# Performance work log

Measured on AMD Instinct MI355X. Metric: run time of the kernel, lower is better.

The kernel has to match this reference:

```python
import jax, jax.numpy as jnp
import numpy as np

# --- fixed model configuration (from init_kwargs) ---
Nx, Nu, Ny, Np = 3, 1, 2, 5
Nz = Np * (Ny + Nu)          # 15
F, V, DELTA = 0.1, 1.0, 1.0  # ps (flow), volume, sampling time
CAMEAN, CBMEAN = 0.5, 0.4    # yscale means
CASTD, CBSTD = 0.3, 0.2      # yscale stds
CAFMEAN, CAFSTD = 1.0, 0.5   # uscale


def _fnn(x, W1, b1, W2, b2):
    # dense(tanh) -> dense(linear), as createDenseLayers/fnnTf
    return jnp.tanh(x @ W1 + b1) @ W2 + b2


def setup_inputs() -> dict:
    B, T = 4096, 1024
    key = jax.random.key(0)
    ks = jax.random.split(key, 16)
    g = lambda k, shp, fan: (jax.random.normal(k, shp, jnp.float32) / np.sqrt(fan))
    return {
        "u": jax.random.normal(ks[0], (B, T, Nu), jnp.float32),
        "xz0": jax.random.normal(ks[1], (B, Nx + Nz), jnp.float32),
        "r1_W1": g(ks[2], (1, 16), 1),  "r1_b1": jnp.zeros((16,), jnp.float32),
        "r1_W2": g(ks[3], (16, 1), 16), "r1_b2": jnp.zeros((1,), jnp.float32),
        "r2_W1": g(ks[4], (2, 16), 2),  "r2_b1": jnp.zeros((16,), jnp.float32),
        "r2_W2": g(ks[5], (16, 1), 16), "r2_b2": jnp.zeros((1,), jnp.float32),
        "eC_W1": g(ks[6], (Nz, 32), Nz), "eC_b1": jnp.zeros((32,), jnp.float32),
        "eC_W2": g(ks[7], (32, 1), 32),  "eC_b2": jnp.zeros((1,), jnp.float32),
    }


def _forward(u, xz0, r1_W1, r1_b1, r1_W2, r1_b2,
             r2_W1, r2_b1, r2_W2, r2_b2, eC_W1, eC_b1, eC_W2, eC_b2):

    def fxu(x, uu):
        Ca, Cb, Cc = x[:, 0:1], x[:, 1:2], x[:, 2:3]
        Caf = uu[:, 0:1]
        r1 = _fnn(Ca, r1_W1, r1_b1, r1_W2, r1_b2) * CASTD
        r2 = _fnn(jnp.concatenate((Cb, Cc), -1), r2_W1, r2_b1, r2_W2, r2_b2) * CBSTD
        Ca = Ca * CASTD + CAMEAN
        Cb = Cb * CBSTD + CBMEAN
        Cc = Cc * CBSTD + CBMEAN
        Caf = Caf * CAFSTD + CAFMEAN
        dCa = F * (Caf - Ca) / V - r1
        dCb = -F * Cb / V + r1 - 3.0 * r2
        dCc = -F * Cc / V + r2
        return jnp.concatenate([dCa / CASTD, dCb / CBSTD, dCc / CBSTD], -1)

    # initial state: replace Cc with NN estimate from past data z0
    y0 = xz0[:, :Ny]
    z0 = xz0[:, Nx:]
    Cc0 = _fnn(z0, eC_W1, eC_b1, eC_W2, eC_b2)
    xz = jnp.concatenate((y0, Cc0, z0), -1)  # [B, Nx+Nz]

    def step(xz, uu):
        x, z = xz[:, :Nx], xz[:, Nx:]
        ypseq, upseq = z[:, :Np * Ny], z[:, Np * Ny:]
        k1 = fxu(x, uu)
        k2 = fxu(x + DELTA * (k1 / 2.0), uu)
        k3 = fxu(x + DELTA * (k2 / 2.0), uu)
        k4 = fxu(x + DELTA * k3, uu)
        xplus = x + (DELTA / 6.0) * (k1 + 2.0 * k2 + 2.0 * k3 + k4)
        zplus = jnp.concatenate((ypseq[:, Ny:], x[:, :Ny], upseq[:, Nu:], uu), -1)
        CcNN = _fnn(z, eC_W1, eC_b1, eC_W2, eC_b2)
        y = jnp.concatenate((x, CcNN), -1)  # [B, Nx+1]
        return jnp.concatenate((xplus, zplus), -1), y

    u_t = jnp.swapaxes(u, 0, 1)  # [T, B, Nu]
    _, ys = jax.lax.scan(step, xz, u_t)
    yseq_full = jnp.swapaxes(ys, 0, 1)      # [B, T, Nx+1]
    yseq = yseq_full[..., :Ny]
    xseq = yseq_full[..., :Nx]
    return yseq_full, yseq, xseq


def reference(u, xz0, r1_W1, r1_b1, r1_W2, r1_b2,
              r2_W1, r2_b1, r2_W2, r2_b2, eC_W1, eC_b1, eC_W2, eC_b2):
    return _forward(u, xz0, r1_W1, r1_b1, r1_W2, r1_b2,
                    r2_W1, r2_b1, r2_W2, r2_b2, eC_W1, eC_b1, eC_W2, eC_b2)
```

## Files before the change

kernel.cpp:

```cpp
#include <hip/hip_runtime.h>
#include <stdint.h>
#include <math.h>

#define NB 4096
#define NT 1024


#if __has_builtin(__builtin_amdgcn_exp2f)
#define EXP2F __builtin_amdgcn_exp2f
#else
#define EXP2F exp2f
#endif
#if __has_builtin(__builtin_amdgcn_rcpf)
#define RCPF __builtin_amdgcn_rcpf
#else
#define RCPF(x) (1.0f / (x))
#endif

#define TANH_SCALE 2.885390081777927f

template <int CTRL>
__device__ __forceinline__ float dppmov(float x) {
  return __int_as_float(
      __builtin_amdgcn_update_dpp(0, __float_as_int(x), CTRL, 0xF, 0xF, true));
}

__device__ __forceinline__ float quadred(float a) {
  a += dppmov<0xB1>(a);
  a += dppmov<0x4E>(a);
  return a;
}

__global__ __launch_bounds__(64) void phase1_kernel(
    const float* __restrict__ u, const float* __restrict__ xz0,
    const float* __restrict__ r1W1, const float* __restrict__ r1b1,
    const float* __restrict__ r1W2, const float* __restrict__ r1b2,
    const float* __restrict__ r2W1, const float* __restrict__ r2b1,
    const float* __restrict__ r2W2, const float* __restrict__ r2b2,
    const float* __restrict__ eCW1, const float* __restrict__ eCb1,
    const float* __restrict__ eCW2, const float* __restrict__ eCb2,
    float* __restrict__ out) {
  const int tid = threadIdx.x;
  const int cl = tid & 7;
  const int q = tid & 3;
  const bool isQ1 = (tid & 4) != 0;
  const int chain = (blockIdx.x << 3) + (tid >> 3);

  float wA[4], wB[4], wC[4], wPn2[4];
  float wPsum = 0.0f;
#pragma unroll
  for (int m = 0; m < 4; ++m) {
    const int un = q + 4 * m;
    float wp;
    if (!isQ1) {
      wA[m] = r1W1[un] * TANH_SCALE;
      wB[m] = 0.0f;
      wC[m] = r1b1[un] * TANH_SCALE;
      wp = r1W2[un];
    } else {
      wA[m] = r2W1[un] * TANH_SCALE;
      wB[m] = r2W1[16 + un] * TANH_SCALE;
      wC[m] = r2b1[un] * TANH_SCALE;
      wp = r2W2[un];
    }
    wPn2[m] = -2.0f * wp;
    wPsum += wp;
  }
  const float c1 = r1b2[0];
  const float c2 = r2b2[0];
  const float C0b = 1.0f / 6.0f - c1;
  const float C1 = -0.2f + 1.5f * c1 - 3.0f * c2;
  const float C2 = c2 - 0.2f;
  const float aO0 = isQ1 ? 0.0f : -1.0f;
  const float aT0 = isQ1 ? -1.0f : 0.0f;
  const float aO1 = isQ1 ? -3.0f : 1.5f;
  const float aT1 = isQ1 ? 1.5f : -3.0f;
  const float aO2 = isQ1 ? 1.0f : 0.0f;
  const float aT2 = isQ1 ? 0.0f : 1.0f;

  const float* xzr = xz0 + chain * 18;
  float x0 = xzr[0];
  float x1 = xzr[1];
  float x2;

  {
    float eh[4], ewn2[4];
    float ewsum = 0.0f;
#pragma unroll
    for (int m = 0; m < 4; ++m) {
      const int un = 4 * cl + m;
      eh[m] = eCb1[un];
      ewn2[m] = -2.0f * eCW2[un];
      ewsum += eCW2[un];
    }
#pragma unroll
    for (int i = 0; i < 15; ++i) {
      const float z = xzr[3 + i];
#pragma unroll
      for (int m = 0; m < 4; ++m)
        eh[m] = __builtin_fmaf(z, eCW1[i * 32 + 4 * cl + m], eh[m]);
    }
    float pl = ewsum;
#pragma unroll
    for (int m = 0; m < 4; ++m) {
      const float e = EXP2F(eh[m] * TANH_SCALE);
      const float r = RCPF(e + 1.0f);
      pl = __builtin_fmaf(ewn2[m], r, pl);
    }
    pl = quadred(pl);
    pl = pl + dppmov<0x141>(pl);
    x2 = pl + eCb2[0];
  }

  size_t idx0;
  int stride;
  if (cl < 3) {
    idx0 = (size_t)chain * NT * 4 + cl;
    stride = 4;
  } else if (cl < 5) {
    idx0 = (size_t)NB * NT * 4 + (size_t)chain * NT * 2 + (cl - 3);
    stride = 2;
  } else {
    idx0 = (size_t)NB * NT * 6 + (size_t)chain * NT * 3 + (cl - 5);
    stride = 3;
  }
  float* sp = out + idx0;
  const bool selx0 = (cl == 0) || (cl == 3) || (cl == 5);
  const bool selx1 = (cl == 1) || (cl == 4) || (cl == 6);

  auto fxu = [&](float s0s, float s1s, float s2s, float C0t, float& k0,
                 float& k1, float& k2) {
    const float sU = isQ1 ? s1s : s0s;
    const float sV = isQ1 ? s2s : s0s;
    float r[4];
#pragma unroll
    for (int m = 0; m < 4; ++m) {
      float h = __builtin_fmaf(sV, wB[m], wC[m]);
      h = __builtin_fmaf(sU, wA[m], h);
      const float e = EXP2F(h);
      r[m] = RCPF(e + 1.0f);
    }
    float pl = wPsum;
#pragma unroll
    for (int m = 0; m < 4; ++m) pl = __builtin_fmaf(wPn2[m], r[m], pl);
    const float Sown = quadred(pl);
    const float Soth = dppmov<0x141>(Sown);
    const float u0 = __builtin_fmaf(-0.1f, s0s, C0t);
    const float u1 = __builtin_fmaf(-0.1f, s1s, C1);
    const float u2 = __builtin_fmaf(-0.1f, s2s, C2);
    k0 = __builtin_fmaf(aO0, Sown, u0);
    k1 = __builtin_fmaf(aO1, Sown, u1);
    k2 = __builtin_fmaf(aO2, Sown, u2);
    k0 = __builtin_fmaf(aT0, Soth, k0);
    k1 = __builtin_fmaf(aT1, Soth, k1);
    k2 = __builtin_fmaf(aT2, Soth, k2);
  };

  const float* urow = u + (size_t)chain * NT;
  float4 ucur = *(const float4*)urow;
  for (int t4 = 0; t4 < NT; t4 += 4) {
    const int tn = (t4 + 4 < NT) ? (t4 + 4) : (NT - 4);
    const float4 unext = *(const float4*)(urow + tn);
    const float us[4] = {ucur.x, ucur.y, ucur.z, ucur.w};
#pragma unroll
    for (int e = 0; e < 4; ++e) {
      const float v = selx0 ? x0 : (selx1 ? x1 : x2);
      *sp = v;
      sp += stride;
      const float C0t = __builtin_fmaf(us[e], 1.0f / 6.0f, C0b);
      float k10, k11, k12, k20, k21, k22, k30, k31, k32, k40, k41, k42;
      fxu(x0, x1, x2, C0t, k10, k11, k12);
      fxu(__builtin_fmaf(0.5f, k10, x0), __builtin_fmaf(0.5f, k11, x1),
          __builtin_fmaf(0.5f, k12, x2), C0t, k20, k21, k22);
      fxu(__builtin_fmaf(0.5f, k20, x0), __builtin_fmaf(0.5f, k21, x1),
          __builtin_fmaf(0.5f, k22, x2), C0t, k30, k31, k32);
      fxu(x0 + k30, x1 + k31, x2 + k32, C0t, k40, k41, k42);
      float tA = k20 + k30;
      tA = __builtin_fmaf(2.0f, tA, k10) + k40;
      x0 = __builtin_fmaf(1.0f / 6.0f, tA, x0);
      float tB = k21 + k31;
      tB = __builtin_fmaf(2.0f, tB, k11) + k41;
      x1 = __builtin_fmaf(1.0f / 6.0f, tB, x1);
      float tC = k22 + k32;
      tC = __builtin_fmaf(2.0f, tC, k12) + k42;
      x2 = __builtin_fmaf(1.0f / 6.0f, tC, x2);
    }
    ucur = unext;
  }
}

__global__ __launch_bounds__(256) void phase2_kernel(
    const float* __restrict__ u, const float* __restrict__ xz0,
    const float* __restrict__ eCW1, const float* __restrict__ eCb1,
    const float* __restrict__ eCW2, const float* __restrict__ eCb2,
    float* __restrict__ out) {
  __shared__ float lw[32][16];
  __shared__ float lw2[32];
  const int tid = threadIdx.x;
  if (tid < 32) {
#pragma unroll
    for (int i = 0; i < 15; ++i) lw[tid][i] = eCW1[i * 32 + tid] * TANH_SCALE;
    lw[tid][15] = eCb1[tid] * TANH_SCALE;
    lw2[tid] = -2.0f * eCW2[tid];
  }
  __syncthreads();

  const int b = blockIdx.x;
  const int t0 = tid << 2;
  const float2* ysrow =
      (const float2*)(out + (size_t)NB * NT * 4) + (size_t)b * NT;
  const float* urow = u + (size_t)b * NT;
  const float* xzr = xz0 + b * 18;

  float yw[16], uw[8];
#pragma unroll
  for (int idx = 0; idx < 8; ++idx) {
    const int tp = t0 - 5 + idx;
    float a, c, uu;
    if (tp >= 0) {
      const float2 h = ysrow[tp];
      a = h.x;
      c = h.y;
      uu = urow[tp];
    } else {
      a = xzr[3 + 2 * (tp + 5)];
      c = xzr[4 + 2 * (tp + 5)];
      uu = xzr[13 + (tp + 5)];
    }
    yw[2 * idx] = a;
    yw[2 * idx + 1] = c;
    uw[idx] = uu;
  }

  float acc[4] = {0.f, 0.f, 0.f, 0.f};
  for (int j = 0; j < 32; ++j) {
    const float4 wa = ((const float4*)lw[j])[0];
    const float4 wb = ((const float4*)lw[j])[1];
    const float4 wc = ((const float4*)lw[j])[2];
    const float4 wd = ((const float4*)lw[j])[3];
    const float w2n = lw2[j];
#pragma unroll
    for (int e = 0; e < 4; ++e) {
      float h = wd.w;
      h = __builtin_fmaf(yw[2 * e + 0], wa.x, h);
      h = __builtin_fmaf(yw[2 * e + 1], wa.y, h);
      h = __builtin_fmaf(yw[2 * e + 2], wa.z, h);
      h = __builtin_fmaf(yw[2 * e + 3], wa.w, h);
      h = __builtin_fmaf(yw[2 * e + 4], wb.x, h);
      h = __builtin_fmaf(yw[2 * e + 5], wb.y, h);
      h = __builtin_fmaf(yw[2 * e + 6], wb.z, h);
      h = __builtin_fmaf(yw[2 * e + 7], wb.w, h);
      h = __builtin_fmaf(yw[2 * e + 8], wc.x, h);
      h = __builtin_fmaf(yw[2 * e + 9], wc.y, h);
      h = __builtin_fmaf(uw[e + 0], wc.z, h);
      h = __builtin_fmaf(uw[e + 1], wc.w, h);
      h = __builtin_fmaf(uw[e + 2], wd.x, h);
      h = __builtin_fmaf(uw[e + 3], wd.y, h);
      h = __builtin_fmaf(uw[e + 4], wd.z, h);
      const float r = RCPF(EXP2F(h) + 1.0f);
      acc[e] = __builtin_fmaf(w2n, r, acc[e]);
    }
  }
  float sw = 0.0f;
#pragma unroll
  for (int j = 0; j < 32; ++j) sw += eCW2[j];
  const float C = eCb2[0] + sw;
  float* yfrow = out + (size_t)b * NT * 4;
#pragma unroll
  for (int e = 0; e < 4; ++e) {
    yfrow[(t0 + e) * 4 + 3] = acc[e] + C;
  }
}

extern "C" void kernel_launch(void* const* d_in, const int* in_sizes, int n_in,
                              void* d_out, int out_size, void* d_ws,
                              size_t ws_size, hipStream_t stream) {
  const float* u = (const float*)d_in[0];
  const float* xz0 = (const float*)d_in[1];
  const float* r1W1 = (const float*)d_in[2];
  const float* r1b1 = (const float*)d_in[3];
  const float* r1W2 = (const float*)d_in[4];
  const float* r1b2 = (const float*)d_in[5];
  const float* r2W1 = (const float*)d_in[6];
  const float* r2b1 = (const float*)d_in[7];
  const float* r2W2 = (const float*)d_in[8];
  const float* r2b2 = (const float*)d_in[9];
  const float* eCW1 = (const float*)d_in[10];
  const float* eCb1 = (const float*)d_in[11];
  const float* eCW2 = (const float*)d_in[12];
  const float* eCb2 = (const float*)d_in[13];
  float* out = (float*)d_out;

  hipLaunchKernelGGL(phase1_kernel, dim3(NB / 8), dim3(64), 0, stream, u, xz0,
                     r1W1, r1b1, r1W2, r1b2, r2W1, r2b1, r2W2, r2b2, eCW1,
                     eCb1, eCW2, eCb2, out);
  hipLaunchKernelGGL(phase2_kernel, dim3(NB), dim3(256), 0, stream, u, xz0,
                     eCW1, eCb1, eCW2, eCb2, out);
}
```

Before: 584.8 us.

## Restructure RK4 stages with incremental hidden-preactivation updates and packed FMA

```diff
diff --git a/kernel.cpp b/kernel.cpp
--- a/kernel.cpp
+++ b/kernel.cpp
@@ -17,18 +17,16 @@
 #define RCPF(x) (1.0f / (x))
 #endif
 
-#define TANH_SCALE 2.885390081777927f
+#define TS 2.885390081777927f
+
+typedef float f32x2 __attribute__((ext_vector_type(2)));
+__device__ __forceinline__ f32x2 sp2(float s) { return (f32x2){s, s}; }
+#define FMA2(a, b, c) __builtin_elementwise_fma((a), (b), (c))
 
 template <int CTRL>
 __device__ __forceinline__ float dppmov(float x) {
   return __int_as_float(
       __builtin_amdgcn_update_dpp(0, __float_as_int(x), CTRL, 0xF, 0xF, true));
-}
-
-__device__ __forceinline__ float quadred(float a) {
-  a += dppmov<0xB1>(a);
-  a += dppmov<0x4E>(a);
-  return a;
 }
 
 __global__ __launch_bounds__(64) void phase1_kernel(
@@ -46,37 +44,58 @@
   const bool isQ1 = (tid & 4) != 0;
   const int chain = (blockIdx.x << 3) + (tid >> 3);
 
-  float wA[4], wB[4], wC[4], wPn2[4];
-  float wPsum = 0.0f;
-#pragma unroll
-  for (int m = 0; m < 4; ++m) {
-    const int un = q + 4 * m;
-    float wp;
-    if (!isQ1) {
-      wA[m] = r1W1[un] * TANH_SCALE;
-      wB[m] = 0.0f;
-      wC[m] = r1b1[un] * TANH_SCALE;
-      wp = r1W2[un];
-    } else {
-      wA[m] = r2W1[un] * TANH_SCALE;
-      wB[m] = r2W1[16 + un] * TANH_SCALE;
-      wC[m] = r2b1[un] * TANH_SCALE;
-      wp = r2W2[un];
-    }
-    wPn2[m] = -2.0f * wp;
-    wPsum += wp;
-  }
+  f32x2 wAv0, wAv1, wBv0, wBv1, wCv0, wCv1, wPn2v0, wPn2v1;
+  float wPsum;
+  {
+    float wa[4], wb[4], wc[4], wp[4];
+#pragma unroll
+    for (int m = 0; m < 4; ++m) {
+      const int un = q + 4 * m;
+      if (!isQ1) {
+        wa[m] = r1W1[un] * TS;
+        wb[m] = 0.0f;
+        wc[m] = r1b1[un] * TS;
+        wp[m] = r1W2[un];
+      } else {
+        wa[m] = r2W1[un] * TS;
+        wb[m] = r2W1[16 + un] * TS;
+        wc[m] = r2b1[un] * TS;
+        wp[m] = r2W2[un];
+      }
+    }
+    wAv0 = (f32x2){wa[0], wa[1]};
+    wAv1 = (f32x2){wa[2], wa[3]};
+    wBv0 = (f32x2){wb[0], wb[1]};
+    wBv1 = (f32x2){wb[2], wb[3]};
+    wCv0 = (f32x2){wc[0], wc[1]};
+    wCv1 = (f32x2){wc[2], wc[3]};
+    wPn2v0 = (f32x2){-2.0f * wp[0], -2.0f * wp[1]};
+    wPn2v1 = (f32x2){-2.0f * wp[2], -2.0f * wp[3]};
+    wPsum = wp[0] + wp[1] + wp[2] + wp[3];
+  }
+  const f32x2 wPh = {wPsum, 0.0f};
+  const f32x2 zero2 = {0.0f, 0.0f};
+
+  const f32x2 cwAh0 = 0.5f * wAv0, cwAh1 = 0.5f * wAv1;
+  const f32x2 cwAf0 = wAv0, cwAf1 = wAv1;
+  const f32x2 cwBh0 = 0.5f * wBv0, cwBh1 = 0.5f * wBv1;
+  const f32x2 cwBf0 = wBv0, cwBf1 = wBv1;
+  const f32x2 eOWNh0 =
+      isQ1 ? (0.5f * wBv0 - 1.5f * wAv0) : (-0.5f * wAv0);
+  const f32x2 eOWNh1 =
+      isQ1 ? (0.5f * wBv1 - 1.5f * wAv1) : (-0.5f * wAv1);
+  const f32x2 eOWNf0 = isQ1 ? (wBv0 - 3.0f * wAv0) : (-wAv0);
+  const f32x2 eOWNf1 = isQ1 ? (wBv1 - 3.0f * wAv1) : (-wAv1);
+  const f32x2 eOTHh0 = isQ1 ? (0.75f * wAv0) : zero2;
+  const f32x2 eOTHh1 = isQ1 ? (0.75f * wAv1) : zero2;
+  const f32x2 eOTHf0 = isQ1 ? (1.5f * wAv0) : zero2;
+  const f32x2 eOTHf1 = isQ1 ? (1.5f * wAv1) : zero2;
+
   const float c1 = r1b2[0];
   const float c2 = r2b2[0];
   const float C0b = 1.0f / 6.0f - c1;
   const float C1 = -0.2f + 1.5f * c1 - 3.0f * c2;
   const float C2 = c2 - 0.2f;
-  const float aO0 = isQ1 ? 0.0f : -1.0f;
-  const float aT0 = isQ1 ? -1.0f : 0.0f;
-  const float aO1 = isQ1 ? -3.0f : 1.5f;
-  const float aT1 = isQ1 ? 1.5f : -3.0f;
-  const float aO2 = isQ1 ? 1.0f : 0.0f;
-  const float aT2 = isQ1 ? 0.0f : 1.0f;
 
   const float* xzr = xz0 + chain * 18;
   float x0 = xzr[0];
@@ -103,11 +122,12 @@
     float pl = ewsum;
 #pragma unroll
     for (int m = 0; m < 4; ++m) {
-      const float e = EXP2F(eh[m] * TANH_SCALE);
+      const float e = EXP2F(eh[m] * TS);
       const float r = RCPF(e + 1.0f);
       pl = __builtin_fmaf(ewn2[m], r, pl);
     }
-    pl = quadred(pl);
+    pl += dppmov<0xB1>(pl);
+    pl += dppmov<0x4E>(pl);
     pl = pl + dppmov<0x141>(pl);
     x2 = pl + eCb2[0];
   }
@@ -128,32 +148,25 @@
   const bool selx0 = (cl == 0) || (cl == 3) || (cl == 5);
   const bool selx1 = (cl == 1) || (cl == 4) || (cl == 6);
 
-  auto fxu = [&](float s0s, float s1s, float s2s, float C0t, float& k0,
-                 float& k1, float& k2) {
-    const float sU = isQ1 ? s1s : s0s;
-    const float sV = isQ1 ? s2s : s0s;
-    float r[4];
-#pragma unroll
-    for (int m = 0; m < 4; ++m) {
-      float h = __builtin_fmaf(sV, wB[m], wC[m]);
-      h = __builtin_fmaf(sU, wA[m], h);
-      const float e = EXP2F(h);
-      r[m] = RCPF(e + 1.0f);
-    }
-    float pl = wPsum;
-#pragma unroll
-    for (int m = 0; m < 4; ++m) pl = __builtin_fmaf(wPn2[m], r[m], pl);
-    const float Sown = quadred(pl);
-    const float Soth = dppmov<0x141>(Sown);
-    const float u0 = __builtin_fmaf(-0.1f, s0s, C0t);
-    const float u1 = __builtin_fmaf(-0.1f, s1s, C1);
-    const float u2 = __builtin_fmaf(-0.1f, s2s, C2);
-    k0 = __builtin_fmaf(aO0, Sown, u0);
-    k1 = __builtin_fmaf(aO1, Sown, u1);
-    k2 = __builtin_fmaf(aO2, Sown, u2);
-    k0 = __builtin_fmaf(aT0, Soth, k0);
-    k1 = __builtin_fmaf(aT1, Soth, k1);
-    k2 = __builtin_fmaf(aT2, Soth, k2);
+  auto nets = [&](f32x2 h0, f32x2 h1, float& Sown, float& Soth) {
+    f32x2 e0, e1, r01, r23;
+    e0.x = EXP2F(h0.x);
+    e0.y = EXP2F(h0.y);
+    e1.x = EXP2F(h1.x);
+    e1.y = EXP2F(h1.y);
+    e0 = e0 + sp2(1.0f);
+    e1 = e1 + sp2(1.0f);
+    r01.x = RCPF(e0.x);
+    r01.y = RCPF(e0.y);
+    r23.x = RCPF(e1.x);
+    r23.y = RCPF(e1.y);
+    f32x2 acc = FMA2(wPn2v0, r01, wPh);
+    acc = FMA2(wPn2v1, r23, acc);
+    float pl = acc.x + acc.y;
+    pl += dppmov<0xB1>(pl);
+    pl += dppmov<0x4E>(pl);
+    Sown = pl;
+    Soth = dppmov<0x141>(pl);
   };
 
   const float* urow = u + (size_t)chain * NT;
@@ -161,20 +174,79 @@
   for (int t4 = 0; t4 < NT; t4 += 4) {
     const int tn = (t4 + 4 < NT) ? (t4 + 4) : (NT - 4);
     const float4 unext = *(const float4*)(urow + tn);
-    const float us[4] = {ucur.x, ucur.y, ucur.z, ucur.w};
+    const float us4[4] = {ucur.x, ucur.y, ucur.z, ucur.w};
 #pragma unroll
     for (int e = 0; e < 4; ++e) {
       const float v = selx0 ? x0 : (selx1 ? x1 : x2);
       *sp = v;
       sp += stride;
-      const float C0t = __builtin_fmaf(us[e], 1.0f / 6.0f, C0b);
-      float k10, k11, k12, k20, k21, k22, k30, k31, k32, k40, k41, k42;
-      fxu(x0, x1, x2, C0t, k10, k11, k12);
-      fxu(__builtin_fmaf(0.5f, k10, x0), __builtin_fmaf(0.5f, k11, x1),
-          __builtin_fmaf(0.5f, k12, x2), C0t, k20, k21, k22);
-      fxu(__builtin_fmaf(0.5f, k20, x0), __builtin_fmaf(0.5f, k21, x1),
-          __builtin_fmaf(0.5f, k22, x2), C0t, k30, k31, k32);
-      fxu(x0 + k30, x1 + k31, x2 + k32, C0t, k40, k41, k42);
+      const float C0t = __builtin_fmaf(us4[e], 1.0f / 6.0f, C0b);
+      const float U0 = __builtin_fmaf(-0.1f, x0, C0t);
+      const float U1 = __builtin_fmaf(-0.1f, x1, C1);
+      const float U2 = __builtin_fmaf(-0.1f, x2, C2);
+      const float sU = isQ1 ? x1 : x0;
+      const float sV = isQ1 ? x2 : x0;
+      const f32x2 hx0 = FMA2(sp2(sU), wAv0, FMA2(sp2(sV), wBv0, wCv0));
+      const f32x2 hx1 = FMA2(sp2(sU), wAv1, FMA2(sp2(sV), wBv1, wCv1));
+      float So, St, S1, S2;
+      nets(hx0, hx1, So, St);
+      S1 = isQ1 ? St : So;
+      S2 = isQ1 ? So : St;
+      const float k10 = U0 - S1;
+      const float k11 =
+          __builtin_fmaf(1.5f, S1, __builtin_fmaf(-3.0f, S2, U1));
+      const float k12 = U2 + S2;
+      {
+        const float Ua = isQ1 ? U1 : U0;
+        const f32x2 p0 = FMA2(cwAh0, sp2(Ua), FMA2(cwBh0, sp2(U2), hx0));
+        const f32x2 p1 = FMA2(cwAh1, sp2(Ua), FMA2(cwBh1, sp2(U2), hx1));
+        const f32x2 h0 = FMA2(eOTHh0, sp2(St), FMA2(eOWNh0, sp2(So), p0));
+        const f32x2 h1 = FMA2(eOTHh1, sp2(St), FMA2(eOWNh1, sp2(So), p1));
+        nets(h0, h1, So, St);
+      }
+      const float U0_2 = __builtin_fmaf(-0.05f, k10, U0);
+      const float U1_2 = __builtin_fmaf(-0.05f, k11, U1);
+      const float U2_2 = __builtin_fmaf(-0.05f, k12, U2);
+      S1 = isQ1 ? St : So;
+      S2 = isQ1 ? So : St;
+      const float k20 = U0_2 - S1;
+      const float k21 =
+          __builtin_fmaf(1.5f, S1, __builtin_fmaf(-3.0f, S2, U1_2));
+      const float k22 = U2_2 + S2;
+      {
+        const float Ua = isQ1 ? U1_2 : U0_2;
+        const f32x2 p0 = FMA2(cwAh0, sp2(Ua), FMA2(cwBh0, sp2(U2_2), hx0));
+        const f32x2 p1 = FMA2(cwAh1, sp2(Ua), FMA2(cwBh1, sp2(U2_2), hx1));
+        const f32x2 h0 = FMA2(eOTHh0, sp2(St), FMA2(eOWNh0, sp2(So), p0));
+        const f32x2 h1 = FMA2(eOTHh1, sp2(St), FMA2(eOWNh1, sp2(So), p1));
+        nets(h0, h1, So, St);
+      }
+      const float U0_3 = __builtin_fmaf(-0.05f, k20, U0);
+      const float U1_3 = __builtin_fmaf(-0.05f, k21, U1);
+      const float U2_3 = __builtin_fmaf(-0.05f, k22, U2);
+      S1 = isQ1 ? St : So;
+      S2 = isQ1 ? So : St;
+      const float k30 = U0_3 - S1;
+      const float k31 =
+          __builtin_fmaf(1.5f, S1, __builtin_fmaf(-3.0f, S2, U1_3));
+      const float k32 = U2_3 + S2;
+      {
+        const float Ua = isQ1 ? U1_3 : U0_3;
+        const f32x2 p0 = FMA2(cwAf0, sp2(Ua), FMA2(cwBf0, sp2(U2_3), hx0));
+        const f32x2 p1 = FMA2(cwAf1, sp2(Ua), FMA2(cwBf1, sp2(U2_3), hx1));
+        const f32x2 h0 = FMA2(eOTHf0, sp2(St), FMA2(eOWNf0, sp2(So), p0));
+        const f32x2 h1 = FMA2(eOTHf1, sp2(St), FMA2(eOWNf1, sp2(So), p1));
+        nets(h0, h1, So, St);
+      }
+      const float U0_4 = __builtin_fmaf(-0.1f, k30, U0);
+      const float U1_4 = __builtin_fmaf(-0.1f, k31, U1);
+      const float U2_4 = __builtin_fmaf(-0.1f, k32, U2);
+      S1 = isQ1 ? St : So;
+      S2 = isQ1 ? So : St;
+      const float k40 = U0_4 - S1;
+      const float k41 =
+          __builtin_fmaf(1.5f, S1, __builtin_fmaf(-3.0f, S2, U1_4));
+      const float k42 = U2_4 + S2;
       float tA = k20 + k30;
       tA = __builtin_fmaf(2.0f, tA, k10) + k40;
       x0 = __builtin_fmaf(1.0f / 6.0f, tA, x0);
@@ -199,8 +271,8 @@
   const int tid = threadIdx.x;
   if (tid < 32) {
 #pragma unroll
-    for (int i = 0; i < 15; ++i) lw[tid][i] = eCW1[i * 32 + tid] * TANH_SCALE;
-    lw[tid][15] = eCb1[tid] * TANH_SCALE;
+    for (int i = 0; i < 15; ++i) lw[tid][i] = eCW1[i * 32 + tid] * TS;
+    lw[tid][15] = eCb1[tid] * TS;
     lw2[tid] = -2.0f * eCW2[tid];
   }
   __syncthreads();
```

Result: no change. 591.7 us (+1.2%).
